# Optimization experiments

Measured on AMD Instinct MI355X. Metric: run time of the kernel, lower is better.

## Reference

```python
import jax, jax.numpy as jnp
import numpy as np

N = 50000      # nodes
E = 800000     # edges (avg degree 16)
IN = 100       # in_channels (hard-coded LayerNorm(100))
H = 128        # hidden_channels
G = 512        # num graphs in batch
C = 2          # num_classes
EPS = 1e-5     # LayerNorm eps (torch default)


def setup_inputs() -> dict:
    key = jax.random.key(0)
    ks = jax.random.split(key, 12)
    x = jax.random.normal(ks[0], (N, IN), dtype=jnp.float32)
    edge_index = jax.random.randint(ks[1], (2, E), 0, N, dtype=jnp.int64)
    edge_weight = jax.random.uniform(ks[2], (E,), dtype=jnp.float32)
    batch = jnp.sort(jax.random.randint(ks[3], (N,), 0, G, dtype=jnp.int64))
    # LayerNorm params (identity init, as torch)
    ln_g0, ln_b0 = jnp.ones((IN,), jnp.float32), jnp.zeros((IN,), jnp.float32)
    ln_g1, ln_b1 = jnp.ones((H,), jnp.float32), jnp.zeros((H,), jnp.float32)
    ln_g2, ln_b2 = jnp.ones((H,), jnp.float32), jnp.zeros((H,), jnp.float32)
    # GCNConv weights (glorot-ish scale) and biases
    W0 = jax.random.normal(ks[4], (IN, H), jnp.float32) / np.float32(np.sqrt(IN))
    b0 = jnp.zeros((H,), jnp.float32)
    W1 = jax.random.normal(ks[5], (H, H), jnp.float32) / np.float32(np.sqrt(H))
    b1 = jnp.zeros((H,), jnp.float32)
    W2 = jax.random.normal(ks[6], (H, H), jnp.float32) / np.float32(np.sqrt(H))
    b2 = jnp.zeros((H,), jnp.float32)
    # Final classifier
    Wlin = jax.random.normal(ks[7], (H, C), jnp.float32) / np.float32(np.sqrt(H))
    blin = jnp.zeros((C,), jnp.float32)
    return {"x": x, "edge_index": edge_index, "edge_weight": edge_weight,
            "batch": batch,
            "ln_g0": ln_g0, "ln_b0": ln_b0, "ln_g1": ln_g1, "ln_b1": ln_b1,
            "ln_g2": ln_g2, "ln_b2": ln_b2,
            "W0": W0, "b0": b0, "W1": W1, "b1": b1, "W2": W2, "b2": b2,
            "Wlin": Wlin, "blin": blin}


def _layernorm(h, g, b):
    m = jnp.mean(h, axis=-1, keepdims=True)
    v = jnp.mean(jnp.square(h - m), axis=-1, keepdims=True)
    return (h - m) * jax.lax.rsqrt(v + EPS) * g + b


def _gcn_conv(h, W, b, src, dst, edge_weight):
    # GCNConv(normalize=False): linear transform, edge gather scaled by
    # edge_weight, scatter-add to destination nodes, plus bias.
    hW = h @ W                                  # [N, H]
    msg = hW[src] * edge_weight[:, None]        # [E, H]
    agg = jax.ops.segment_sum(msg, dst, num_segments=N)  # [N, H]
    return agg + b


def reference(x, edge_index, edge_weight, batch,
              ln_g0, ln_b0, ln_g1, ln_b1, ln_g2, ln_b2,
              W0, b0, W1, b1, W2, b2, Wlin, blin):
    src, dst = edge_index[0], edge_index[1]
    layers = [(ln_g0, ln_b0, W0, b0), (ln_g1, ln_b1, W1, b1), (ln_g2, ln_b2, W2, b2)]
    h = x
    for (g, bb, W, cb) in layers:
        h = _layernorm(h, g, bb)
        h = _gcn_conv(h, W, cb, src, dst, edge_weight)
        h = jax.nn.relu(h)  # dropout is identity in eval mode
    # global mean pool over graphs
    sums = jax.ops.segment_sum(h, batch, num_segments=G)                       # [G, H]
    cnt = jax.ops.segment_sum(jnp.ones((N, 1), h.dtype), batch, num_segments=G)
    pooled = sums / jnp.maximum(cnt, 1.0)
    return pooled @ Wlin + blin  # [G, C]
```

## Files before the change

kernel.cpp:

```cpp
#include <hip/hip_runtime.h>
#include <hip/hip_bf16.h>

#define NN 50000
#define NE 800000
#define NG 512
#define HD 128
#define EPS 1e-5f
#define L1B 196
#define EPB 4096
#define NL1 ((NE + EPB - 1) / EPB)

typedef __attribute__((ext_vector_type(8))) short short8;
typedef __attribute__((ext_vector_type(4))) float f32x4;

__device__ __forceinline__ float bfu(unsigned short u) {
    return __uint_as_float((unsigned)u << 16);
}

__global__ __launch_bounds__(256) void k_zero(int* __restrict__ gtot,
                                              float* __restrict__ pooled) {
    const int i = blockIdx.x * 256 + threadIdx.x;
    if (i < L1B) gtot[i] = 0;
    if (i < NG * HD) pooled[i] = 0.f;
}

__global__ __launch_bounds__(256) void k_histL1(const int* __restrict__ dstv,
                                                int* __restrict__ gtot, int E) {
    __shared__ int h[L1B];
    const int t  = threadIdx.x;
    const int e0 = blockIdx.x * EPB;
    const int e1 = (e0 + EPB < E) ? (e0 + EPB) : E;
    for (int i = t; i < L1B; i += 256) h[i] = 0;
    __syncthreads();
    for (int e = e0 + t; e < e1; e += 256) atomicAdd(&h[dstv[e] >> 8], 1);
    __syncthreads();
    for (int i = t; i < L1B; i += 256)
        if (h[i]) atomicAdd(&gtot[i], h[i]);
}

__global__ __launch_bounds__(256) void k_scan196(const int* __restrict__ gtot,
                                                 int* __restrict__ gbase,
                                                 int* __restrict__ gcursor,
                                                 int* __restrict__ row_ptr) {
    __shared__ int s[256];
    const int t = threadIdx.x;
    const int v = (t < L1B) ? gtot[t] : 0;
    s[t] = v;
    __syncthreads();
    for (int off = 1; off < 256; off <<= 1) {
        int u = (t >= off) ? s[t - off] : 0;
        __syncthreads();
        s[t] += u;
        __syncthreads();
    }
    const int ex = s[t] - v;
    if (t < L1B) { gbase[t] = ex; gcursor[t] = ex; }
    if (t == 0) { gbase[L1B] = NE; row_ptr[NN] = NE; }
}

__global__ __launch_bounds__(256) void k_binL1(const int* __restrict__ srcv,
                                               const int* __restrict__ dstv,
                                               const float* __restrict__ ewt,
                                               int* __restrict__ gcursor,
                                               int2* __restrict__ stage, int E) {
    __shared__ int hist[L1B], lstart[L1B], gbase[L1B], lcur[L1B];
    __shared__ int s[256];
    __shared__ int2 lsort[EPB];
    const int t  = threadIdx.x;
    const int e0 = blockIdx.x * EPB;
    const int e1 = (e0 + EPB < E) ? (e0 + EPB) : E;
    for (int i = t; i < L1B; i += 256) hist[i] = 0;
    __syncthreads();
    for (int e = e0 + t; e < e1; e += 256)
        atomicAdd(&hist[dstv[e] >> 8], 1);
    __syncthreads();
    {
        const int v = (t < L1B) ? hist[t] : 0;
        s[t] = v;
        __syncthreads();
        for (int off = 1; off < 256; off <<= 1) {
            int u = (t >= off) ? s[t - off] : 0;
            __syncthreads();
            s[t] += u;
            __syncthreads();
        }
        if (t < L1B) {
            const int ex = s[t] - v;
            lstart[t] = ex;
            lcur[t]   = ex;
            gbase[t]  = v ? atomicAdd(&gcursor[t], v) : 0;
        }
    }
    __syncthreads();
    for (int e = e0 + t; e < e1; e += 256) {
        const int d = dstv[e];
        const int r = atomicAdd(&lcur[d >> 8], 1);
        lsort[r] = make_int2((d << 16) | srcv[e], __float_as_int(ewt[e]));
    }
    __syncthreads();
    const int n = e1 - e0;
    for (int i = t; i < n; i += 256) {
        const int2 el = lsort[i];
        const unsigned b = ((unsigned)el.x) >> 24;
        stage[gbase[b] + (i - lstart[b])] = el;
    }
}

__global__ __launch_bounds__(256) void k_binL2(const int2* __restrict__ stage,
                                               const int* __restrict__ gbase,
                                               int* __restrict__ row_ptr,
                                               int2* __restrict__ cw) {
    __shared__ int cnt[256], s[256], cur[256];
    const int t    = threadIdx.x;
    const int b    = blockIdx.x;
    const int d0   = b << 8;
    const int nd   = (NN - d0 < 256) ? (NN - d0) : 256;
    const int base = gbase[b];
    const int end  = gbase[b + 1];
    cnt[t] = 0;
    __syncthreads();
    for (int i = base + t; i < end; i += 256) {
        const unsigned dst = ((unsigned)stage[i].x) >> 16;
        atomicAdd(&cnt[dst - d0], 1);
    }
    __syncthreads();
    {
        const int v = cnt[t];
        s[t] = v;
        __syncthreads();
        for (int off = 1; off < 256; off <<= 1) {
            int u = (t >= off) ? s[t - off] : 0;
            __syncthreads();
            s[t] += u;
            __syncthreads();
        }
        const int ex = base + s[t] - v;
        cur[t] = ex;
        if (t < nd) row_ptr[d0 + t] = ex;
    }
    __syncthreads();
    for (int i = base + t; i < end; i += 256) {
        const int2 el = stage[i];
        const unsigned dst = ((unsigned)el.x) >> 16;
        const int p = atomicAdd(&cur[dst - d0], 1);
        cw[p] = make_int2(el.x & 0xFFFF, el.y);
    }
}

__global__ __launch_bounds__(256) void k_wpack(const float* __restrict__ W0,
                                               const float* __restrict__ W1,
                                               const float* __restrict__ W2,
                                               __hip_bfloat16* __restrict__ bp) {
    const int tg    = blockIdx.x * 256 + threadIdx.x;
    const int layer = tg >> 11;
    const int f     = tg & 2047;
    const int tile  = f >> 8, kk = (f >> 6) & 3, lane = f & 63;
    const int col   = tile * 16 + (lane & 15);
    const int kbase = kk * 32 + ((lane >> 4) << 3);
    const float* W  = (layer == 0) ? W0 : (layer == 1) ? W1 : W2;
    const int Klim  = (layer == 0) ? 100 : 128;
    alignas(16) __hip_bfloat16 o[8];
#pragma unroll
    for (int j = 0; j < 8; ++j) {
        const int k = kbase + j;
        o[j] = __float2bfloat16((k < Klim) ? W[(size_t)k * HD + col] : 0.f);
    }
    *(float4*)&bp[(size_t)tg * 8] = *(const float4*)o;
}

__device__ __forceinline__ void mfma_gemm_store(const __hip_bfloat16 (*hb)[136],
                                                const __hip_bfloat16* __restrict__ bp,
                                                __hip_bfloat16* __restrict__ hwb,
                                                int t, int r0) {
    const int wave = t >> 6, lane = t & 63;
    const int rw   = wave * 16;
    const int arow = rw + (lane & 15);
    const int acol = ((lane >> 4) << 3);
    short8 a[4];
#pragma unroll
    for (int kk = 0; kk < 4; ++kk)
        a[kk] = *(const short8*)&hb[arow][kk * 32 + acol];

    f32x4 acc[8] = {};
    const short8* bfr = (const short8*)bp;
#pragma unroll
    for (int tile = 0; tile < 8; ++tile) {
#pragma unroll
        for (int kk = 0; kk < 4; ++kk) {
            const short8 bb = bfr[(tile * 4 + kk) * 64 + lane];
            acc[tile] = __builtin_amdgcn_mfma_f32_16x16x32_bf16(a[kk], bb, acc[tile], 0, 0, 0);
        }
    }
    const int baser = r0 + rw + ((lane >> 4) << 2);
    const int bcol  = lane & 15;
#pragma unroll
    for (int tile = 0; tile < 8; ++tile) {
        const int col = tile * 16 + bcol;
#pragma unroll
        for (int j = 0; j < 4; ++j) {
            const int row = baser + j;
            if (row < NN) hwb[(size_t)row * HD + col] = __float2bfloat16(acc[tile][j]);
        }
    }
}

__global__ __launch_bounds__(256, 3) void k_ln_gemm_f32(const float* __restrict__ hin,
                                                        const float* __restrict__ g,
                                                        const float* __restrict__ b,
                                                        const __hip_bfloat16* __restrict__ bp,
                                                        __hip_bfloat16* __restrict__ hwb) {
    constexpr int K  = 100;
    constexpr int SK = K + 4;
    __shared__ float hs[64][SK];
    __shared__ __hip_bfloat16 hb[64][136];
    const int t  = threadIdx.x;
    const int r0 = blockIdx.x * 64;
    {
        const float4* src4 = (const float4*)(hin + (size_t)r0 * K);
        const int valid_rows = (NN - r0 < 64) ? (NN - r0) : 64;
        const int maxf = valid_rows * K;
        for (int i = t; i < 64 * K / 4; i += 256) {
            int f = i * 4;
            float4 v = (f < maxf) ? src4[i] : make_float4(0.f, 0.f, 0.f, 0.f);
            int r = f / K, k = f - r * K;
            *(float4*)&hs[r][k] = v;
        }
    }
    __syncthreads();
    {
        const int row = t >> 2, l = t & 3;
        float s = 0.f, s2 = 0.f;
        for (int k = l; k < K; k += 4) { float v = hs[row][k]; s += v; s2 += v * v; }
        s  += __shfl_xor(s, 1);  s2 += __shfl_xor(s2, 1);
        s  += __shfl_xor(s, 2);  s2 += __shfl_xor(s2, 2);
        const float mean = s / (float)K;
        const float var  = s2 / (float)K - mean * mean;
        const float rstd = rsqrtf(var + EPS);
        for (int k = l; k < K; k += 4)
            hb[row][k] = __float2bfloat16((hs[row][k] - mean) * rstd * g[k] + b[k]);
        for (int k = K + l; k < 128; k += 4)
            hb[row][k] = __float2bfloat16(0.f);
    }
    __syncthreads();
    mfma_gemm_store(hb, bp, hwb, t, r0);
}

__global__ __launch_bounds__(256, 4) void k_ln_gemm_b16(const __hip_bfloat16* __restrict__ hin,
                                                        const float* __restrict__ g,
                                                        const float* __restrict__ b,
                                                        const __hip_bfloat16* __restrict__ bp,
                                                        __hip_bfloat16* __restrict__ hwb) {
    __shared__ __hip_bfloat16 hb[64][136];
    const int t  = threadIdx.x;
    const int r0 = blockIdx.x * 64;
    {
        const float4* src4 = (const float4*)(hin + (size_t)r0 * HD);
        const int valid_rows = (NN - r0 < 64) ? (NN - r0) : 64;
        const int maxv = valid_rows * 16;
        for (int i = t; i < 1024; i += 256) {
            float4 v = (i < maxv) ? src4[i] : make_float4(0.f, 0.f, 0.f, 0.f);
            const int r = i >> 4, k = (i & 15) * 8;
            *(float4*)&hb[r][k] = v;
        }
    }
    __syncthreads();
    {
        const int row = t >> 2, l = t & 3;
        float s = 0.f, s2 = 0.f;
        for (int k = l; k < 128; k += 4) {
            const float v = __bfloat162float(hb[row][k]);
            s += v; s2 += v * v;
        }
        s  += __shfl_xor(s, 1);  s2 += __shfl_xor(s2, 1);
        s  += __shfl_xor(s, 2);  s2 += __shfl_xor(s2, 2);
        const float mean = s / 128.f;
        const float var  = s2 / 128.f - mean * mean;
        const float rstd = rsqrtf(var + EPS);
        for (int k = l; k < 128; k += 4)
            hb[row][k] = __float2bfloat16((__bfloat162float(hb[row][k]) - mean) * rstd * g[k] + b[k]);
    }
    __syncthreads();
    mfma_gemm_store(hb, bp, hwb, t, r0);
}

__device__ __forceinline__ float4 agg_row(const __hip_bfloat16* __restrict__ hwb,
                                          const int2* __restrict__ cw,
                                          const float* __restrict__ bias,
                                          int e0, int e1, size_t coff) {
    float4 acc = {0.f, 0.f, 0.f, 0.f};
    int e = e0;
    for (; e + 8 <= e1; e += 8) {
        int2 c[8];
#pragma unroll
        for (int j = 0; j < 8; ++j) c[j] = cw[e + j];
        ushort4 r[8];
#pragma unroll
        for (int j = 0; j < 8; ++j)
            r[j] = *(const ushort4*)(hwb + (size_t)c[j].x * HD + coff);
#pragma unroll
        for (int j = 0; j < 8; ++j) {
            const float w = __int_as_float(c[j].y);
            acc.x += w * bfu(r[j].x);
            acc.y += w * bfu(r[j].y);
            acc.z += w * bfu(r[j].z);
            acc.w += w * bfu(r[j].w);
        }
    }
    if (e + 4 <= e1) {
        int2 c[4];
#pragma unroll
        for (int j = 0; j < 4; ++j) c[j] = cw[e + j];
        ushort4 r[4];
#pragma unroll
        for (int j = 0; j < 4; ++j)
            r[j] = *(const ushort4*)(hwb + (size_t)c[j].x * HD + coff);
#pragma unroll
        for (int j = 0; j < 4; ++j) {
            const float w = __int_as_float(c[j].y);
            acc.x += w * bfu(r[j].x);
            acc.y += w * bfu(r[j].y);
            acc.z += w * bfu(r[j].z);
            acc.w += w * bfu(r[j].w);
        }
        e += 4;
    }
    for (; e < e1; ++e) {
        const int2 c = cw[e];
        const float w = __int_as_float(c.y);
        const ushort4 rv = *(const ushort4*)(hwb + (size_t)c.x * HD + coff);
        acc.x += w * bfu(rv.x);
        acc.y += w * bfu(rv.y);
        acc.z += w * bfu(rv.z);
        acc.w += w * bfu(rv.w);
    }
    const float4 bb = *(const float4*)(bias + coff);
    float4 o;
    o.x = fmaxf(acc.x + bb.x, 0.f);
    o.y = fmaxf(acc.y + bb.y, 0.f);
    o.z = fmaxf(acc.z + bb.z, 0.f);
    o.w = fmaxf(acc.w + bb.w, 0.f);
    return o;
}

__global__ __launch_bounds__(256) void k_aggregate(const __hip_bfloat16* __restrict__ hwb,
                                                   const int* __restrict__ row_ptr,
                                                   const int2* __restrict__ cw,
                                                   const float* __restrict__ bias,
                                                   __hip_bfloat16* __restrict__ hout, int n) {
    const int t    = threadIdx.x;
    const int grp  = t >> 5;
    const int lane = t & 31;
    const int node = blockIdx.x * 8 + grp;
    if (node >= n) return;
    const size_t coff = (size_t)lane * 4;
    float4 o = agg_row(hwb, cw, bias, row_ptr[node], row_ptr[node + 1], coff);
    alignas(8) __hip_bfloat16 ob[4] = {
        __float2bfloat16(o.x), __float2bfloat16(o.y),
        __float2bfloat16(o.z), __float2bfloat16(o.w)};
    *(ushort4*)(hout + (size_t)node * HD + coff) = *(const ushort4*)ob;
}

__global__ __launch_bounds__(256) void k_aggpool(const __hip_bfloat16* __restrict__ hwb,
                                                 const int* __restrict__ row_ptr,
                                                 const int2* __restrict__ cw,
                                                 const float* __restrict__ bias,
                                                 const int* __restrict__ batch,
                                                 float* __restrict__ pooled, int n) {
    __shared__ float lds[8][128];
    __shared__ int gof[8];
    const int t    = threadIdx.x;
    const int grp  = t >> 5;
    const int lane = t & 31;
    const int node = blockIdx.x * 8 + grp;
    const size_t coff = (size_t)lane * 4;
    float4 o = {0.f, 0.f, 0.f, 0.f};
    if (node < n)
        o = agg_row(hwb, cw, bias, row_ptr[node], row_ptr[node + 1], coff);
    *(float4*)&lds[grp][lane * 4] = o;
    if (lane == 0) gof[grp] = (node < n) ? batch[node] : -1;
    __syncthreads();
    if (t < 128) {
        float sum = 0.f;
        int curg = gof[0];
#pragma unroll
        for (int r = 0; r < 8; ++r) {
            const int gr = gof[r];
            if (gr != curg) {
                if (curg >= 0) atomicAdd(&pooled[curg * HD + t], sum);
                sum = 0.f;
                curg = gr;
            }
            if (gr >= 0) sum += lds[r][t];
        }
        if (curg >= 0) atomicAdd(&pooled[curg * HD + t], sum);
    }
}

__global__ __launch_bounds__(128) void k_linout(const float* __restrict__ pooled,
                                                const int* __restrict__ batch,
                                                const float* __restrict__ Wlin,
                                                const float* __restrict__ blin,
                                                float* __restrict__ out, int n) {
    __shared__ float red[2][128];
    const int gph = blockIdx.x;
    const int c   = threadIdx.x;
    int lo = 0, hi = n;
    while (lo < hi) { int mid = (lo + hi) >> 1; if (batch[mid] < gph) lo = mid + 1; else hi = mid; }
    const int start = lo;
    hi = n;
    while (lo < hi) { int mid = (lo + hi) >> 1; if (batch[mid] < gph + 1) lo = mid + 1; else hi = mid; }
    const float cnt = (float)(lo - start);
    const float pv = pooled[gph * HD + c] / fmaxf(cnt, 1.0f);
    red[0][c] = pv * Wlin[c * 2 + 0];
    red[1][c] = pv * Wlin[c * 2 + 1];
    __syncthreads();
    for (int off = 64; off; off >>= 1) {
        if (c < off) { red[0][c] += red[0][c + off]; red[1][c] += red[1][c + off]; }
        __syncthreads();
    }
    if (c == 0) {
        out[gph * 2 + 0] = red[0][0] + blin[0];
        out[gph * 2 + 1] = red[1][0] + blin[1];
    }
}

extern "C" void kernel_launch(void* const* d_in, const int* in_sizes, int n_in,
                              void* d_out, int out_size, void* d_ws, size_t ws_size,
                              hipStream_t stream) {
    const float* x     = (const float*)d_in[0];
    const int*   ei    = (const int*)d_in[1];
    const float* ewt   = (const float*)d_in[2];
    const int*   batch = (const int*)d_in[3];
    const float* ln_g0 = (const float*)d_in[4];
    const float* ln_b0 = (const float*)d_in[5];
    const float* ln_g1 = (const float*)d_in[6];
    const float* ln_b1 = (const float*)d_in[7];
    const float* ln_g2 = (const float*)d_in[8];
    const float* ln_b2 = (const float*)d_in[9];
    const float* W0    = (const float*)d_in[10];
    const float* b0    = (const float*)d_in[11];
    const float* W1    = (const float*)d_in[12];
    const float* b1    = (const float*)d_in[13];
    const float* W2    = (const float*)d_in[14];
    const float* b2    = (const float*)d_in[15];
    const float* Wlin  = (const float*)d_in[16];
    const float* blin  = (const float*)d_in[17];
    float* out = (float*)d_out;

    const int* srcv = ei;
    const int* dstv = ei + NE;

    char* ws = (char*)d_ws;
    size_t o = 0;
    auto carve = [&](size_t bytes) { void* p = ws + o; o += (bytes + 255) & ~(size_t)255; return p; };
    int*   row_ptr = (int*)carve(sizeof(int) * (NN + 1));
    int*   gtot    = (int*)carve(sizeof(int) * L1B);
    int*   gbase   = (int*)carve(sizeof(int) * (L1B + 1));
    int*   gcursor = (int*)carve(sizeof(int) * L1B);
    float* pooled  = (float*)carve(sizeof(float) * NG * HD);
    int2*  cw      = (int2*)carve(sizeof(int2) * NE);
    int2*  stage   = (int2*)carve(sizeof(int2) * NE);
    __hip_bfloat16* bpack = (__hip_bfloat16*)carve(sizeof(__hip_bfloat16) * 3 * 2048 * 8);
    __hip_bfloat16* hwb   = (__hip_bfloat16*)carve(sizeof(__hip_bfloat16) * NN * HD);
    __hip_bfloat16* hA    = (__hip_bfloat16*)carve(sizeof(__hip_bfloat16) * NN * HD);
    __hip_bfloat16* hB    = (__hip_bfloat16*)carve(sizeof(__hip_bfloat16) * NN * HD);
    (void)ws_size; (void)n_in; (void)in_sizes; (void)out_size;

    k_zero<<<256, 256, 0, stream>>>(gtot, pooled);
    k_wpack<<<(3 * 2048) / 256, 256, 0, stream>>>(W0, W1, W2, bpack);

    k_histL1<<<NL1, 256, 0, stream>>>(dstv, gtot, NE);
    k_scan196<<<1, 256, 0, stream>>>(gtot, gbase, gcursor, row_ptr);
    k_binL1<<<NL1, 256, 0, stream>>>(srcv, dstv, ewt, gcursor, stage, NE);
    k_binL2<<<L1B, 256, 0, stream>>>(stage, gbase, row_ptr, cw);

    const int GEMM_GRID = (NN + 63) / 64;
    const int AGG_GRID  = (NN + 7) / 8;

    k_ln_gemm_f32<<<GEMM_GRID, 256, 0, stream>>>(x, ln_g0, ln_b0, bpack, hwb);
    k_aggregate<<<AGG_GRID, 256, 0, stream>>>(hwb, row_ptr, cw, b0, hA, NN);
    k_ln_gemm_b16<<<GEMM_GRID, 256, 0, stream>>>(hA, ln_g1, ln_b1, bpack + 2048 * 8, hwb);
    k_aggregate<<<AGG_GRID, 256, 0, stream>>>(hwb, row_ptr, cw, b1, hB, NN);
    k_ln_gemm_b16<<<GEMM_GRID, 256, 0, stream>>>(hB, ln_g2, ln_b2, bpack + 2 * 2048 * 8, hwb);
    k_aggpool<<<AGG_GRID, 256, 0, stream>>>(hwb, row_ptr, cw, b2, batch, pooled, NN);
    k_linout<<<NG, 128, 0, stream>>>(pooled, batch, Wlin, blin, out, NN);
}
```

Baseline: 210.9 us.

## Pack CSR edges into 32-bit src+bf16 weight, widen gather unroll, fuse init kernels

Compresses each CSR entry from an 8-byte (src, fp32 weight) pair to a 4-byte word holding a 16-bit source index and a bf16 edge weight. This halves edge-list traffic in the three aggregation passes. The gather loop is unrolled to 16 edges with nontemporal loads to expose more memory parallelism, and the weight-packing kernel is merged into the zeroing kernel to drop one launch. The 16-bit source field only holds values up to 65535, which covers N=50000. Rounding edge weights to bf16 adds numerical error.

After: 237.3 us. 12.5% more time.

```diff
diff --git a/kernel.cpp b/kernel.cpp
--- a/kernel.cpp
+++ b/kernel.cpp
@@ -17,11 +17,31 @@
     return __uint_as_float((unsigned)u << 16);
 }
 
-__global__ __launch_bounds__(256) void k_zero(int* __restrict__ gtot,
-                                              float* __restrict__ pooled) {
+__global__ __launch_bounds__(256) void k_init(int* __restrict__ gtot,
+                                              float* __restrict__ pooled,
+                                              const float* __restrict__ W0,
+                                              const float* __restrict__ W1,
+                                              const float* __restrict__ W2,
+                                              __hip_bfloat16* __restrict__ bp) {
     const int i = blockIdx.x * 256 + threadIdx.x;
     if (i < L1B) gtot[i] = 0;
     if (i < NG * HD) pooled[i] = 0.f;
+    if (i < 3 * 2048) {
+        const int layer = i >> 11;
+        const int f     = i & 2047;
+        const int tile  = f >> 8, kk = (f >> 6) & 3, lane = f & 63;
+        const int col   = tile * 16 + (lane & 15);
+        const int kbase = kk * 32 + ((lane >> 4) << 3);
+        const float* W  = (layer == 0) ? W0 : (layer == 1) ? W1 : W2;
+        const int Klim  = (layer == 0) ? 100 : 128;
+        alignas(16) __hip_bfloat16 o[8];
+#pragma unroll
+        for (int j = 0; j < 8; ++j) {
+            const int k = kbase + j;
+            o[j] = __float2bfloat16((k < Klim) ? W[(size_t)k * HD + col] : 0.f);
+        }
+        *(float4*)&bp[(size_t)i * 8] = *(const float4*)o;
+    }
 }
 
 __global__ __launch_bounds__(256) void k_histL1(const int* __restrict__ dstv,
@@ -109,7 +129,7 @@
 __global__ __launch_bounds__(256) void k_binL2(const int2* __restrict__ stage,
                                                const int* __restrict__ gbase,
                                                int* __restrict__ row_ptr,
-                                               int2* __restrict__ cw) {
+                                               unsigned* __restrict__ cw) {
     __shared__ int cnt[256], s[256], cur[256];
     const int t    = threadIdx.x;
     const int b    = blockIdx.x;
@@ -143,29 +163,10 @@
         const int2 el = stage[i];
         const unsigned dst = ((unsigned)el.x) >> 16;
         const int p = atomicAdd(&cur[dst - d0], 1);
-        cw[p] = make_int2(el.x & 0xFFFF, el.y);
-    }
-}
-
-__global__ __launch_bounds__(256) void k_wpack(const float* __restrict__ W0,
-                                               const float* __restrict__ W1,
-                                               const float* __restrict__ W2,
-                                               __hip_bfloat16* __restrict__ bp) {
-    const int tg    = blockIdx.x * 256 + threadIdx.x;
-    const int layer = tg >> 11;
-    const int f     = tg & 2047;
-    const int tile  = f >> 8, kk = (f >> 6) & 3, lane = f & 63;
-    const int col   = tile * 16 + (lane & 15);
-    const int kbase = kk * 32 + ((lane >> 4) << 3);
-    const float* W  = (layer == 0) ? W0 : (layer == 1) ? W1 : W2;
-    const int Klim  = (layer == 0) ? 100 : 128;
-    alignas(16) __hip_bfloat16 o[8];
-#pragma unroll
-    for (int j = 0; j < 8; ++j) {
-        const int k = kbase + j;
-        o[j] = __float2bfloat16((k < Klim) ? W[(size_t)k * HD + col] : 0.f);
-    }
-    *(float4*)&bp[(size_t)tg * 8] = *(const float4*)o;
+        __hip_bfloat16 hw16 = __float2bfloat16(__int_as_float(el.y));
+        const unsigned wb = *reinterpret_cast<const unsigned short*>(&hw16);
+        cw[p] = (((unsigned)el.x & 0xFFFFu) << 16) | wb;
+    }
 }
 
 __device__ __forceinline__ void mfma_gemm_store(const __hip_bfloat16 (*hb)[136],
@@ -284,50 +285,68 @@
 }
 
 __device__ __forceinline__ float4 agg_row(const __hip_bfloat16* __restrict__ hwb,
-                                          const int2* __restrict__ cw,
+                                          const unsigned* __restrict__ cw,
                                           const float* __restrict__ bias,
                                           int e0, int e1, size_t coff) {
     float4 acc = {0.f, 0.f, 0.f, 0.f};
     int e = e0;
-    for (; e + 8 <= e1; e += 8) {
-        int2 c[8];
-#pragma unroll
-        for (int j = 0; j < 8; ++j) c[j] = cw[e + j];
-        ushort4 r[8];
-#pragma unroll
-        for (int j = 0; j < 8; ++j)
-            r[j] = *(const ushort4*)(hwb + (size_t)c[j].x * HD + coff);
-#pragma unroll
-        for (int j = 0; j < 8; ++j) {
-            const float w = __int_as_float(c[j].y);
+    for (; e + 16 <= e1; e += 16) {
+        unsigned c[16];
+#pragma unroll
+        for (int j = 0; j < 16; ++j) c[j] = __builtin_nontemporal_load(&cw[e + j]);
+        ushort4 r[16];
+#pragma unroll
+        for (int j = 0; j < 16; ++j)
+            r[j] = *(const ushort4*)(hwb + (size_t)(c[j] >> 16) * HD + coff);
+#pragma unroll
+        for (int j = 0; j < 16; ++j) {
+            const float w = bfu((unsigned short)(c[j] & 0xFFFFu));
             acc.x += w * bfu(r[j].x);
             acc.y += w * bfu(r[j].y);
             acc.z += w * bfu(r[j].z);
             acc.w += w * bfu(r[j].w);
         }
     }
-    if (e + 4 <= e1) {
-        int2 c[4];
-#pragma unroll
-        for (int j = 0; j < 4; ++j) c[j] = cw[e + j];
-        ushort4 r[4];
-#pragma unroll
-        for (int j = 0; j < 4; ++j)
-            r[j] = *(const ushort4*)(hwb + (size_t)c[j].x * HD + coff);
-#pragma unroll
-        for (int j = 0; j < 4; ++j) {
-            const float w = __int_as_float(c[j].y);
+    if (e + 8 <= e1) {
+        unsigned c[8];
+#pragma unroll
+        for (int j = 0; j < 8; ++j) c[j] = __builtin_nontemporal_load(&cw[e + j]);
+        ushort4 r[8];
+#pragma unroll
+        for (int j = 0; j < 8; ++j)
+            r[j] = *(const ushort4*)(hwb + (size_t)(c[j] >> 16) * HD + coff);
+#pragma unroll
+        for (int j = 0; j < 8; ++j) {
+            const float w = bfu((unsigned short)(c[j] & 0xFFFFu));
             acc.x += w * bfu(r[j].x);
             acc.y += w * bfu(r[j].y);
             acc.z += w * bfu(r[j].z);
             acc.w += w * bfu(r[j].w);
         }
+        e += 8;
+    }
+    if (e + 4 <= e1) {
+        unsigned c[4];
+#pragma unroll
+        for (int j = 0; j < 4; ++j) c[j] = __builtin_nontemporal_load(&cw[e + j]);
+        ushort4 r[4];
+#pragma unroll
+        for (int j = 0; j < 4; ++j)
+            r[j] = *(const ushort4*)(hwb + (size_t)(c[j] >> 16) * HD + coff);
+#pragma unroll
+        for (int j = 0; j < 4; ++j) {
+            const float w = bfu((unsigned short)(c[j] & 0xFFFFu));
+            acc.x += w * bfu(r[j].x);
+            acc.y += w * bfu(r[j].y);
+            acc.z += w * bfu(r[j].z);
+            acc.w += w * bfu(r[j].w);
+        }
         e += 4;
     }
     for (; e < e1; ++e) {
-        const int2 c = cw[e];
-        const float w = __int_as_float(c.y);
-        const ushort4 rv = *(const ushort4*)(hwb + (size_t)c.x * HD + coff);
+        const unsigned c = cw[e];
+        const float w = bfu((unsigned short)(c & 0xFFFFu));
+        const ushort4 rv = *(const ushort4*)(hwb + (size_t)(c >> 16) * HD + coff);
         acc.x += w * bfu(rv.x);
         acc.y += w * bfu(rv.y);
         acc.z += w * bfu(rv.z);
@@ -344,7 +363,7 @@
 
 __global__ __launch_bounds__(256) void k_aggregate(const __hip_bfloat16* __restrict__ hwb,
                                                    const int* __restrict__ row_ptr,
-                                                   const int2* __restrict__ cw,
+                                                   const unsigned* __restrict__ cw,
                                                    const float* __restrict__ bias,
                                                    __hip_bfloat16* __restrict__ hout, int n) {
     const int t    = threadIdx.x;
@@ -362,7 +381,7 @@
 
 __global__ __launch_bounds__(256) void k_aggpool(const __hip_bfloat16* __restrict__ hwb,
                                                  const int* __restrict__ row_ptr,
-                                                 const int2* __restrict__ cw,
+                                                 const unsigned* __restrict__ cw,
                                                  const float* __restrict__ bias,
                                                  const int* __restrict__ batch,
                                                  float* __restrict__ pooled, int n) {
@@ -453,21 +472,20 @@
     char* ws = (char*)d_ws;
     size_t o = 0;
     auto carve = [&](size_t bytes) { void* p = ws + o; o += (bytes + 255) & ~(size_t)255; return p; };
-    int*   row_ptr = (int*)carve(sizeof(int) * (NN + 1));
-    int*   gtot    = (int*)carve(sizeof(int) * L1B);
-    int*   gbase   = (int*)carve(sizeof(int) * (L1B + 1));
-    int*   gcursor = (int*)carve(sizeof(int) * L1B);
-    float* pooled  = (float*)carve(sizeof(float) * NG * HD);
-    int2*  cw      = (int2*)carve(sizeof(int2) * NE);
-    int2*  stage   = (int2*)carve(sizeof(int2) * NE);
+    int*      row_ptr = (int*)carve(sizeof(int) * (NN + 1));
+    int*      gtot    = (int*)carve(sizeof(int) * L1B);
+    int*      gbase   = (int*)carve(sizeof(int) * (L1B + 1));
+    int*      gcursor = (int*)carve(sizeof(int) * L1B);
+    float*    pooled  = (float*)carve(sizeof(float) * NG * HD);
+    unsigned* cw      = (unsigned*)carve(sizeof(unsigned) * NE);
+    int2*     stage   = (int2*)carve(sizeof(int2) * NE);
     __hip_bfloat16* bpack = (__hip_bfloat16*)carve(sizeof(__hip_bfloat16) * 3 * 2048 * 8);
     __hip_bfloat16* hwb   = (__hip_bfloat16*)carve(sizeof(__hip_bfloat16) * NN * HD);
     __hip_bfloat16* hA    = (__hip_bfloat16*)carve(sizeof(__hip_bfloat16) * NN * HD);
     __hip_bfloat16* hB    = (__hip_bfloat16*)carve(sizeof(__hip_bfloat16) * NN * HD);
     (void)ws_size; (void)n_in; (void)in_sizes; (void)out_size;
 
-    k_zero<<<256, 256, 0, stream>>>(gtot, pooled);
-    k_wpack<<<(3 * 2048) / 256, 256, 0, stream>>>(W0, W1, W2, bpack);
+    k_init<<<257, 256, 0, stream>>>(gtot, pooled, W0, W1, W2, bpack);
 
     k_histL1<<<NL1, 256, 0, stream>>>(dstv, gtot, NE);
     k_scan196<<<1, 256, 0, stream>>>(gtot, gbase, gcursor, row_ptr);
```
